# Performance work log

Measured on AMD Instinct MI355X. Metric: run time of the kernel, lower is better.

## Reference

```python
import jax, jax.numpy as jnp
import numpy as np

SIG = [1, 1, 1, 1, -1]  # Cl(4,1)
NVEC = 5
GA = 1 << NVEC  # 32


def _build_gp_table():
    # Cayley table for the geometric product on blades indexed by bitmask.
    G = np.zeros((GA, GA, GA), np.float32)
    for a in range(GA):
        for b in range(GA):
            s = 0
            t = a >> 1
            while t:
                s += bin(t & b).count('1')
                t >>= 1
            sign = -1.0 if (s & 1) else 1.0
            common = a & b
            for i in range(NVEC):
                if (common >> i) & 1:
                    sign *= SIG[i]
            G[a, b, a ^ b] = sign
    return G

GP_TABLE = jnp.asarray(_build_gp_table())


def geometric_product(x, y):
    return jnp.einsum('...i,...j,ijk->...k', x, y, GP_TABLE)


def manifold_norm(x):
    # normalize each multivector onto the unit sphere in R^32
    return x / (jnp.linalg.norm(x, axis=-1, keepdims=True) + 1e-6)


def versor_linear(x, W, b):
    # channel mixing shared across multivector components: x [..., in, ga]
    return jnp.einsum('...ig,oi->...og', x, W) + b


def layer_norm2d(x, w, b):
    # LayerNorm over last two dims [D, ga] jointly
    mu = jnp.mean(x, axis=(-2, -1), keepdims=True)
    var = jnp.var(x, axis=(-2, -1), keepdims=True)
    return (x - mu) / jnp.sqrt(var + 1e-5) * w + b


def attention(x, Wq, bq, Wk, bk, Wv, bv, Wo, bo, n_heads):
    B, S, D, G = x.shape
    dh = D // n_heads
    q = versor_linear(x, Wq, bq).reshape(B, S, n_heads, dh, G)
    k = versor_linear(x, Wk, bk).reshape(B, S, n_heads, dh, G)
    v = versor_linear(x, Wv, bv).reshape(B, S, n_heads, dh, G)
    scale = 1.0 / np.sqrt(dh * G).astype(np.float32)
    scores = jnp.einsum('bshdg,bthdg->bhst', q, k) * scale
    probs = jax.nn.softmax(scores, axis=-1)
    o = jnp.einsum('bhst,bthdg->bshdg', probs, v).reshape(B, S, D, G)
    return versor_linear(o, Wo, bo)


N_HEADS = 8


def forward(x, Wq, bq, Wk, bk, Wv, bv, Wo, bo, ln1_w, ln1_b, ln2_w, ln2_b,
            gamma1, gamma2, W1, b1, W2, b2, Wr, br, Wc, bc):
    L = Wq.shape[0]
    for l in range(L):
        h = attention(layer_norm2d(x, ln1_w[l], ln1_b[l]),
                      Wq[l], bq[l], Wk[l], bk[l], Wv[l], bv[l], Wo[l], bo[l], N_HEADS)
        x = manifold_norm(x + gamma1[l] * h)
        m = versor_linear(layer_norm2d(x, ln2_w[l], ln2_b[l]), W1[l], b1[l])
        m = versor_linear(jnp.tanh(m), W2[l], b2[l])
        x = manifold_norm(x + gamma2[l] * m)
    # RecursiveRotorAccumulator: log(S)-step inclusive scan of rotors
    delta = versor_linear(x, Wr, br)
    rot = 0.5 * delta
    rot = rot.at[..., 0].add(1.0)
    rot = manifold_norm(rot)
    S = x.shape[1]
    step = 1
    while step < S:
        left = rot[:, :-step]
        right = rot[:, step:]
        comb = manifold_norm(geometric_product(right, left))
        rot = jnp.concatenate([rot[:, :step], comb], axis=1)
        step *= 2
    pooled = rot[:, -1]  # [B, D, ga]
    logits = pooled.reshape(pooled.shape[0], -1) @ Wc.T + bc
    return logits


def setup_inputs() -> dict:
    key = jax.random.key(0)
    B, S, D, G, L, NC = 8, 256, 64, GA, 4, 1000
    E = 4 * D  # expansion hidden
    ks = jax.random.split(key, 16)
    sd = 0.02
    inp = {
        'x': jax.random.normal(ks[0], (B, S, D, G), jnp.float32),
        'Wq': jax.random.normal(ks[1], (L, D, D), jnp.float32) * sd,
        'bq': jnp.zeros((L, D, G), jnp.float32),
        'Wk': jax.random.normal(ks[2], (L, D, D), jnp.float32) * sd,
        'bk': jnp.zeros((L, D, G), jnp.float32),
        'Wv': jax.random.normal(ks[3], (L, D, D), jnp.float32) * sd,
        'bv': jnp.zeros((L, D, G), jnp.float32),
        'Wo': jax.random.normal(ks[4], (L, D, D), jnp.float32) * sd,
        'bo': jnp.zeros((L, D, G), jnp.float32),
        'ln1_w': jnp.ones((L, D, G), jnp.float32),
        'ln1_b': jnp.zeros((L, D, G), jnp.float32),
        'ln2_w': jnp.ones((L, D, G), jnp.float32),
        'ln2_b': jnp.zeros((L, D, G), jnp.float32),
        'gamma1': 1e-5 * jnp.ones((L, D, G), jnp.float32),
        'gamma2': 1e-5 * jnp.ones((L, D, G), jnp.float32),
        'W1': jax.random.normal(ks[5], (L, E, D), jnp.float32) * sd,
        'b1': jnp.zeros((L, E, G), jnp.float32),
        'W2': jax.random.normal(ks[6], (L, D, E), jnp.float32) * sd,
        'b2': jnp.zeros((L, D, G), jnp.float32),
        'Wr': jax.random.normal(ks[7], (D, D), jnp.float32) * sd,
        'br': jnp.zeros((D, G), jnp.float32),
        'Wc': jax.random.normal(ks[8], (NC, D * G), jnp.float32) * sd,
        'bc': jnp.zeros((NC,), jnp.float32),
    }
    return inp


def reference(x, Wq, bq, Wk, bk, Wv, bv, Wo, bo, ln1_w, ln1_b, ln2_w, ln2_b,
              gamma1, gamma2, W1, b1, W2, b2, Wr, br, Wc, bc):
    return forward(x, Wq, bq, Wk, bk, Wv, bv, Wo, bo, ln1_w, ln1_b, ln2_w, ln2_b,
                   gamma1, gamma2, W1, b1, W2, b2, Wr, br, Wc, bc)
```

## Files before the change

kernel.cpp:

```cpp
#include <hip/hip_runtime.h>
#include <hip/hip_bf16.h>

constexpr int kB  = 8;
constexpr int kS  = 256;
constexpr int kD  = 64;
constexpr int kG  = 32;
constexpr int kE  = 256;
constexpr int kNH = 8;
constexpr int kHD = 256;
constexpr int kDG = kD * kG;
constexpr int kT  = kB * kS;
constexpr int kNC = 1000;

using bf16x8 = __attribute__((ext_vector_type(8))) short;
using f32x4  = __attribute__((ext_vector_type(4))) float;

__device__ __forceinline__ short f2bf(float f) {
    unsigned u = __float_as_uint(f);
    unsigned r = (u + 0x7FFFu + ((u >> 16) & 1u)) >> 16;
    return (short)r;
}

__device__ __forceinline__ float tanh_fast(float x) {
    float a = fabsf(x);
    float e = __expf(-2.f * a);
    float d = 1.f + e;
    float r = __builtin_amdgcn_rcpf(d);
    r = r * (2.f - d * r);
    float t = (1.f - e) * r;
    return copysignf(t, x);
}

__global__ __launch_bounds__(256) void cvtw_kernel(
    const float* __restrict__ Wq, const float* __restrict__ Wk,
    const float* __restrict__ Wv, const float* __restrict__ Wo,
    const float* __restrict__ W1, const float* __restrict__ W2,
    unsigned short* __restrict__ dst) {
    int idx = (blockIdx.x * 256 + threadIdx.x) * 4;
    const float* src; int off;
    if      (idx <  16384) { src = Wq; off = 0; }
    else if (idx <  32768) { src = Wk; off = 16384; }
    else if (idx <  49152) { src = Wv; off = 32768; }
    else if (idx <  65536) { src = Wo; off = 49152; }
    else if (idx < 131072) { src = W1; off = 65536; }
    else                   { src = W2; off = 131072; }
    const float4 v = *(const float4*)(src + (idx - off));
    *(short4*)&dst[idx] = make_short4(f2bf(v.x), f2bf(v.y), f2bf(v.z), f2bf(v.w));
}

__global__ __launch_bounds__(256) void prep_tr_kernel(
    const float* __restrict__ bq, const float* __restrict__ bk,
    const float* __restrict__ bv, const float* __restrict__ bo,
    const float* __restrict__ b2, const float* __restrict__ gm1,
    const float* __restrict__ gm2, const float* __restrict__ ln2w,
    const float* __restrict__ ln2b, const float* __restrict__ ln1w,
    const float* __restrict__ ln1b, const float* __restrict__ b1,
    float* __restrict__ dst) {
    __shared__ float lt[32 * 257];
    const int a = blockIdx.x >> 2, l = blockIdx.x & 3;
    const float* srcs[12] = {bq, bk, bv, bo, b2, gm1, gm2, ln2w, ln2b, ln1w, ln1b, b1};
    const int R  = (a == 11) ? 256 : 64;
    const int sh = (a == 11) ? 8 : 6;
    const float* src = srcs[a] + (size_t)l * R * 32;
    float* out = dst + a * 8192 + l * R * 32;
    const int tid = threadIdx.x;
    for (int j = tid; j < R * 32; j += 256) lt[(j & 31) * (R + 1) + (j >> 5)] = src[j];
    __syncthreads();
    for (int k = tid; k < R * 32; k += 256) {
        int g = k >> sh, r = k & (R - 1);
        out[k] = lt[g * (R + 1) + r];
    }
}

__global__ __launch_bounds__(256) void ln_kernel(const float* __restrict__ Xin,
                                                 const float* __restrict__ w,
                                                 const float* __restrict__ b,
                                                 unsigned short* __restrict__ A,
                                                 float* __restrict__ XT) {
    int t = blockIdx.x, tid = threadIdx.x;
    const float* xp = Xin + (size_t)t * kDG;
    __shared__ float r1[256], r2[256];
    __shared__ short st[32 * 72];
    __shared__ float xf[32 * 68];
    float v[8], s = 0.f, ss = 0.f;
#pragma unroll
    for (int j = 0; j < 8; j++) {
        float x = xp[tid + j * 256];
        v[j] = x; s += x; ss += x * x;
        int jj = tid + j * 256;
        xf[(jj & 31) * 68 + (jj >> 5)] = x;
    }
    r1[tid] = s; r2[tid] = ss; __syncthreads();
    for (int o = 128; o > 0; o >>= 1) {
        if (tid < o) { r1[tid] += r1[tid + o]; r2[tid] += r2[tid + o]; }
        __syncthreads();
    }
    float mean = r1[0] * (1.f / kDG);
    float var  = r2[0] * (1.f / kDG) - mean * mean;
    float rstd = rsqrtf(var + 1e-5f);
#pragma unroll
    for (int j = 0; j < 8; j++) {
        int jj = tid + j * 256;
        float val = (v[j] - mean) * rstd * w[jj] + b[jj];
        st[(jj & 31) * 72 + (jj >> 5)] = f2bf(val);
    }
    __syncthreads();
    bf16x8 ov = *(const bf16x8*)&st[(tid >> 3) * 72 + (tid & 7) * 8];
    *(bf16x8*)&A[(size_t)t * kDG + tid * 8] = ov;
    const int row = tid >> 3, col = (tid & 7) * 8;
    float* xo = XT + (size_t)t * kDG + tid * 8;
    *(float4*)(xo + 0) = *(const float4*)&xf[row * 68 + col + 0];
    *(float4*)(xo + 4) = *(const float4*)&xf[row * 68 + col + 4];
}

__global__ __launch_bounds__(256) void vlinT_kernel(const float* __restrict__ XT,
                                                    const float* __restrict__ W,
                                                    const float* __restrict__ bias,
                                                    float* __restrict__ OutT) {
    __shared__ float sx[32 * 65];
    __shared__ float sw[kD * kD];
    int t = blockIdx.x, tid = threadIdx.x;
    const float* xp = XT + (size_t)t * kDG;
    for (int j = tid; j < kDG; j += 256) sx[(j >> 6) * 65 + (j & 63)] = xp[j];
    for (int j = tid; j < kD * kD; j += 256) sw[j] = W[j];
    __syncthreads();
    int g = tid & 31, ob = tid >> 5;
    int b = t >> 8, s = t & 255;
    float* op = OutT + ((size_t)b * kD * kS + s) * kG;
    for (int o = ob; o < kD; o += 8) {
        float acc = bias[o * kG + g];
        const float* wr = sw + o * kD;
#pragma unroll
        for (int i = 0; i < kD; i++) acc += wr[i] * sx[g * 65 + i];
        op[(size_t)o * kS * kG + g] = acc;
    }
}

template<bool LAST>
__global__ __launch_bounds__(256, 2) void mega_kernel(
    const unsigned short* __restrict__ O,
    const unsigned short* __restrict__ Woh, const float* __restrict__ boT,
    const float* __restrict__ gm1T,
    const float* __restrict__ ln2wT, const float* __restrict__ ln2bT,
    const unsigned short* __restrict__ W1h, const float* __restrict__ b1T,
    const unsigned short* __restrict__ W2h, const float* __restrict__ b2T,
    const float* __restrict__ gm2T,
    const float* __restrict__ ln1wT, const float* __restrict__ ln1bT,
    float* __restrict__ XT,
    const unsigned short* __restrict__ Wqh, const unsigned short* __restrict__ Wkh,
    const unsigned short* __restrict__ Wvh,
    const float* __restrict__ bqT, const float* __restrict__ bkT,
    const float* __restrict__ bvT,
    unsigned short* __restrict__ Q, unsigned short* __restrict__ K,
    unsigned short* __restrict__ V) {
    constexpr int AS = 72;
    constexpr int MS = 264;
    __shared__ short sA[32 * AS];
    __shared__ short sM[32 * MS];
    __shared__ float sred[8];

    const int tid = threadIdx.x;
    const int w = tid >> 6, lane = tid & 63;
    const int l16 = lane & 15, quad = lane >> 4;
    const int tok = blockIdx.x;
    const size_t tb = (size_t)tok * kDG;
    const int o0 = w * 16 + quad * 4;

    float xv[2][4];
    bf16x8 w1f[8];
    {
        const unsigned short* xp = O + tb;
        bf16x8 bfr[2][2];
#pragma unroll
        for (int c = 0; c < 2; ++c)
#pragma unroll
            for (int nt = 0; nt < 2; ++nt)
                bfr[c][nt] = *(const bf16x8*)&xp[(nt * 16 + l16) * kD + c * 32 + quad * 8];

        f32x4 accW[2];
#pragma unroll
        for (int nt = 0; nt < 2; ++nt) accW[nt] = (f32x4){0.f, 0.f, 0.f, 0.f};
#pragma unroll
        for (int c = 0; c < 2; ++c) {
            bf16x8 afr = *(const bf16x8*)&Woh[(w * 16 + l16) * kD + c * 32 + quad * 8];
#pragma unroll
            for (int nt = 0; nt < 2; ++nt)
                accW[nt] = __builtin_amdgcn_mfma_f32_16x16x32_bf16(afr, bfr[c][nt], accW[nt], 0, 0, 0);
        }

#pragma unroll
        for (int mt = 0; mt < 4; ++mt)
#pragma unroll
            for (int c = 0; c < 2; ++c)
                w1f[mt * 2 + c] = *(const bf16x8*)&W1h[((w * 4 + mt) * 16 + l16) * kD + c * 32 + quad * 8];

        float4 lw2[2], lb2[2];
#pragma unroll
        for (int nt = 0; nt < 2; ++nt) {
            int g = nt * 16 + l16;
            lw2[nt] = *(const float4*)&ln2wT[g * kD + o0];
            lb2[nt] = *(const float4*)&ln2bT[g * kD + o0];
        }

        float s = 0.f, ss = 0.f;
        float vv[2][4];
#pragma unroll
        for (int nt = 0; nt < 2; ++nt) {
            int g = nt * 16 + l16;
            const float4 b4 = *(const float4*)&boT[g * kD + o0];
            const float4 g4 = *(const float4*)&gm1T[g * kD + o0];
            const float4 xi = *(const float4*)&XT[tb + g * kD + o0];
#pragma unroll
            for (int r = 0; r < 4; ++r)
                vv[nt][r] = (&xi.x)[r] + (&g4.x)[r] * (accW[nt][r] + (&b4.x)[r]);
        }
#pragma unroll
        for (int r = 0; r < 4; ++r) {
            float sq = vv[0][r] * vv[0][r] + vv[1][r] * vv[1][r];
#pragma unroll
            for (int off = 1; off < 16; off <<= 1) sq += __shfl_xor(sq, off, 64);
            float rn = 1.f / (sqrtf(sq) + 1e-6f);
#pragma unroll
            for (int nt = 0; nt < 2; ++nt) {
                float x = vv[nt][r] * rn;
                xv[nt][r] = x;
                s += x; ss = fmaf(x, x, ss);
            }
        }
#pragma unroll
        for (int off = 1; off < 64; off <<= 1) {
            s += __shfl_xor(s, off, 64); ss += __shfl_xor(ss, off, 64);
        }
        if (lane == 0) { sred[w] = s; sred[4 + w] = ss; }
        __syncthreads();
        float st = sred[0] + sred[1] + sred[2] + sred[3];
        float sst = sred[4] + sred[5] + sred[6] + sred[7];
        float mean = st * (1.f / kDG);
        float var  = sst * (1.f / kDG) - mean * mean;
        float rstd = rsqrtf(var + 1e-5f);
#pragma unroll
        for (int nt = 0; nt < 2; ++nt) {
            int g = nt * 16 + l16;
            short4 s4;
#pragma unroll
            for (int r = 0; r < 4; ++r)
                (&s4.x)[r] = f2bf((xv[nt][r] - mean) * rstd * (&lw2[nt].x)[r] + (&lb2[nt].x)[r]);
            *(short4*)&sA[g * AS + o0] = s4;
        }
    }
    __syncthreads();

    bf16x8 w2f[8];
    {
        bf16x8 afrA[2][2];
#pragma unroll
        for (int c = 0; c < 2; ++c)
#pragma unroll
            for (int nt = 0; nt < 2; ++nt)
                afrA[c][nt] = *(const bf16x8*)&sA[(nt * 16 + l16) * AS + c * 32 + quad * 8];

        f32x4 acc1[4][2];
#pragma unroll
        for (int mt = 0; mt < 4; ++mt)
#pragma unroll
            for (int nt = 0; nt < 2; ++nt) acc1[mt][nt] = (f32x4){0.f, 0.f, 0.f, 0.f};
#pragma unroll
        for (int mt = 0; mt < 4; ++mt)
#pragma unroll
            for (int c = 0; c < 2; ++c)
#pragma unroll
                for (int nt = 0; nt < 2; ++nt)
                    acc1[mt][nt] = __builtin_amdgcn_mfma_f32_16x16x32_bf16(w1f[mt * 2 + c], afrA[c][nt], acc1[mt][nt], 0, 0, 0);

#pragma unroll
        for (int c = 0; c < 8; ++c)
            w2f[c] = *(const bf16x8*)&W2h[(w * 16 + l16) * kE + c * 32 + quad * 8];

#pragma unroll
        for (int mt = 0; mt < 4; ++mt)
#pragma unroll
            for (int nt = 0; nt < 2; ++nt) {
                int g = nt * 16 + l16;
                int e0 = (w * 4 + mt) * 16 + quad * 4;
                const float4 b4 = *(const float4*)&b1T[g * kE + e0];
                short4 s4;
#pragma unroll
                for (int r = 0; r < 4; ++r)
                    (&s4.x)[r] = f2bf(tanh_fast(acc1[mt][nt][r] + (&b4.x)[r]));
                *(short4*)&sM[g * MS + e0] = s4;
            }
    }
    __syncthreads();

    f32x4 acc2[2];
#pragma unroll
    for (int nt = 0; nt < 2; ++nt) acc2[nt] = (f32x4){0.f, 0.f, 0.f, 0.f};
#pragma unroll
    for (int c = 0; c < 8; ++c) {
        bf16x8 bq[2];
#pragma unroll
        for (int nt = 0; nt < 2; ++nt)
            bq[nt] = *(const bf16x8*)&sM[(nt * 16 + l16) * MS + c * 32 + quad * 8];
#pragma unroll
        for (int nt = 0; nt < 2; ++nt)
            acc2[nt] = __builtin_amdgcn_mfma_f32_16x16x32_bf16(w2f[c], bq[nt], acc2[nt], 0, 0, 0);
    }

    bf16x8 wqf[6];
    float4 lw1[2], lb1[2], pbq[2], pbk[2], pbv[2];
    if constexpr (!LAST) {
        const unsigned short* Wp[3] = {Wqh, Wkh, Wvh};
#pragma unroll
        for (int m = 0; m < 3; ++m)
#pragma unroll
            for (int c = 0; c < 2; ++c)
                wqf[m * 2 + c] = *(const bf16x8*)&Wp[m][(w * 16 + l16) * kD + c * 32 + quad * 8];
#pragma unroll
        for (int nt = 0; nt < 2; ++nt) {
            int g = nt * 16 + l16;
            lw1[nt] = *(const float4*)&ln1wT[g * kD + o0];
            lb1[nt] = *(const float4*)&ln1bT[g * kD + o0];
            pbq[nt] = *(const float4*)&bqT[g * kD + o0];
            pbk[nt] = *(const float4*)&bkT[g * kD + o0];
            pbv[nt] = *(const float4*)&bvT[g * kD + o0];
        }
    }

    float yv[2][4];
    float s2 = 0.f, ss2 = 0.f;
    {
        float vv[2][4];
#pragma unroll
        for (int nt = 0; nt < 2; ++nt) {
            int g = nt * 16 + l16;
            const float4 b4 = *(const float4*)&b2T[g * kD + o0];
            const float4 g4 = *(const float4*)&gm2T[g * kD + o0];
#pragma unroll
            for (int r = 0; r < 4; ++r)
                vv[nt][r] = xv[nt][r] + (&g4.x)[r] * (acc2[nt][r] + (&b4.x)[r]);
        }
#pragma unroll
        for (int r = 0; r < 4; ++r) {
            float sq = vv[0][r] * vv[0][r] + vv[1][r] * vv[1][r];
#pragma unroll
            for (int off = 1; off < 16; off <<= 1) sq += __shfl_xor(sq, off, 64);
            float rn = 1.f / (sqrtf(sq) + 1e-6f);
#pragma unroll
            for (int nt = 0; nt < 2; ++nt) {
                float x = vv[nt][r] * rn;
                yv[nt][r] = x;
                s2 += x; ss2 = fmaf(x, x, ss2);
            }
        }
#pragma unroll
        for (int nt = 0; nt < 2; ++nt) {
            int g = nt * 16 + l16;
            float4 xo;
#pragma unroll
            for (int r = 0; r < 4; ++r) (&xo.x)[r] = yv[nt][r];
            *(float4*)&XT[tb + g * kD + o0] = xo;
        }
    }
    if constexpr (LAST) return;

#pragma unroll
    for (int off = 1; off < 64; off <<= 1) {
        s2 += __shfl_xor(s2, off, 64); ss2 += __shfl_xor(ss2, off, 64);
    }
    if (lane == 0) { sred[w] = s2; sred[4 + w] = ss2; }
    __syncthreads();
    {
        float st = sred[0] + sred[1] + sred[2] + sred[3];
        float sst = sred[4] + sred[5] + sred[6] + sred[7];
        float mean = st * (1.f / kDG);
        float var  = sst * (1.f / kDG) - mean * mean;
        float rstd = rsqrtf(var + 1e-5f);
#pragma unroll
        for (int nt = 0; nt < 2; ++nt) {
            int g = nt * 16 + l16;
            short4 s4;
#pragma unroll
            for (int r = 0; r < 4; ++r)
                (&s4.x)[r] = f2bf((yv[nt][r] - mean) * rstd * (&lw1[nt].x)[r] + (&lb1[nt].x)[r]);
            *(short4*)&sA[g * AS + o0] = s4;
        }
    }
    __syncthreads();

    {
        bf16x8 afrA[2][2];
#pragma unroll
        for (int c = 0; c < 2; ++c)
#pragma unroll
            for (int nt = 0; nt < 2; ++nt)
                afrA[c][nt] = *(const bf16x8*)&sA[(nt * 16 + l16) * AS + c * 32 + quad * 8];

        const float4* Bp[3][2] = {{&pbq[0], &pbq[1]}, {&pbk[0], &pbk[1]}, {&pbv[0], &pbv[1]}};
        unsigned short* Op[3] = {Q, K, V};
#pragma unroll
        for (int m = 0; m < 3; ++m) {
            f32x4 acc3[2];
#pragma unroll
            for (int nt = 0; nt < 2; ++nt) acc3[nt] = (f32x4){0.f, 0.f, 0.f, 0.f};
#pragma unroll
            for (int c = 0; c < 2; ++c)
#pragma unroll
                for (int nt = 0; nt < 2; ++nt)
                    acc3[nt] = __builtin_amdgcn_mfma_f32_16x16x32_bf16(wqf[m * 2 + c], afrA[c][nt], acc3[nt], 0, 0, 0);
            unsigned short* op = Op[m] + tb;
#pragma unroll
            for (int nt = 0; nt < 2; ++nt) {
                int g = nt * 16 + l16;
                const float4 b4 = *Bp[m][nt];
#pragma unroll
                for (int r = 0; r < 4; ++r)
                    op[(o0 + r) * kG + g] = (unsigned short)f2bf(acc3[nt][r] + (&b4.x)[r]);
            }
        }
    }
}

__global__ __launch_bounds__(256, 3) void gemm_qkv_kernel(
    const unsigned short* __restrict__ X,
    const unsigned short* __restrict__ Wqh, const unsigned short* __restrict__ Wkh,
    const unsigned short* __restrict__ Wvh,
    const float* __restrict__ bqT, const float* __restrict__ bkT, const float* __restrict__ bvT,
    unsigned short* __restrict__ Q, unsigned short* __restrict__ K, unsigned short* __restrict__ V) {
    constexpr int WS = 64 + 8;
    __shared__ short sW[3 * 64 * WS];

    const int tid = threadIdx.x, wave = tid >> 6, lane = tid & 63;
    const int l16 = lane & 15, quad = lane >> 4;
    const int tok = blockIdx.x * 4 + wave;

    const unsigned short* Wp[3] = {Wqh, Wkh, Wvh};
#pragma unroll
    for (int w = 0; w < 3; ++w)
        for (int j = tid * 8; j < 64 * 64; j += 2048) {
            int o = j >> 6, i = j & 63;
            *(bf16x8*)&sW[w * 64 * WS + o * WS + i] = *(const bf16x8*)(Wp[w] + j);
        }

    const unsigned short* xp = X + (size_t)tok * kDG;
    bf16x8 bfr[2][2];
#pragma unroll
    for (int c = 0; c < 2; ++c)
#pragma unroll
        for (int nt = 0; nt < 2; ++nt)
            bfr[c][nt] = *(const bf16x8*)&xp[(nt * 16 + l16) * kD + c * 32 + quad * 8];
    __syncthreads();

    f32x4 acc[3][4][2];
#pragma unroll
    for (int w = 0; w < 3; ++w)
#pragma unroll
        for (int mt = 0; mt < 4; ++mt)
#pragma unroll
            for (int nt = 0; nt < 2; ++nt) acc[w][mt][nt] = (f32x4){0.f, 0.f, 0.f, 0.f};

#pragma unroll
    for (int w = 0; w < 3; ++w)
#pragma unroll
        for (int mt = 0; mt < 4; ++mt)
#pragma unroll
            for (int c = 0; c < 2; ++c) {
                bf16x8 afr = *(const bf16x8*)&sW[w * 64 * WS + (mt * 16 + l16) * WS + c * 32 + quad * 8];
#pragma unroll
                for (int nt = 0; nt < 2; ++nt)
                    acc[w][mt][nt] = __builtin_amdgcn_mfma_f32_16x16x32_bf16(afr, bfr[c][nt], acc[w][mt][nt], 0, 0, 0);
            }

    unsigned short* Op[3] = {Q, K, V};
    const float* Bp[3] = {bqT, bkT, bvT};
#pragma unroll
    for (int w = 0; w < 3; ++w) {
        unsigned short* op = Op[w] + (size_t)tok * kDG;
#pragma unroll
        for (int mt = 0; mt < 4; ++mt)
#pragma unroll
            for (int nt = 0; nt < 2; ++nt) {
                int g = nt * 16 + l16;
                int o0 = mt * 16 + quad * 4;
                const float4 b4 = *(const float4*)&Bp[w][g * kD + o0];
#pragma unroll
                for (int r = 0; r < 4; ++r)
                    op[(o0 + r) * kG + g] = (unsigned short)f2bf(acc[w][mt][nt][r] + (&b4.x)[r]);
            }
    }
}

constexpr int QSTR = 264;
constexpr int VSTR = 40;

__global__ __launch_bounds__(128) void attn_mfma_kernel(const unsigned short* __restrict__ Q,
                                                        const unsigned short* __restrict__ K,
                                                        const unsigned short* __restrict__ V,
                                                        unsigned short* __restrict__ O) {
    __shared__ short sP[32 * QSTR];
    __shared__ short sKV[2][256 * VSTR];

    const int qt = blockIdx.x, h = blockIdx.y, b = blockIdx.z;
    const int tid = threadIdx.x;
    const int wave = tid >> 6, lane = tid & 63;
    const int l16 = lane & 15, quad = lane >> 4;

    const size_t bh = (size_t)b * kS * kDG + (size_t)h * kHD;

    bf16x8 afrag[8];
    {
        const unsigned short* qp = Q + bh + (size_t)(qt * 32 + wave * 16 + l16) * kDG;
#pragma unroll
        for (int c = 0; c < 8; ++c)
            afrag[c] = *(const bf16x8*)(qp + c * 32 + quad * 8);
    }

#pragma unroll
    for (int it = 0; it < 8; ++it) {
        int j = it * 1024 + tid * 8;
        int row = j >> 8, col = j & 255;
        *(bf16x8*)&sKV[0][row * QSTR + col] =
            *(const bf16x8*)(K + bh + (size_t)row * kDG + col);
    }
    __syncthreads();

    f32x4 acc[16];
#pragma unroll
    for (int i = 0; i < 16; ++i) acc[i] = (f32x4){0.f, 0.f, 0.f, 0.f};

    for (int kt = 0; kt < 8; ++kt) {
        bf16x8 kpre[8];
        if (kt < 7) {
#pragma unroll
            for (int it = 0; it < 8; ++it) {
                int j = it * 1024 + tid * 8;
                int row = j >> 8, col = j & 255;
                kpre[it] = *(const bf16x8*)(K + bh + (size_t)((kt + 1) * 32 + row) * kDG + col);
            }
        }
        const short* kb = sKV[kt & 1];
#pragma unroll
        for (int nt = 0; nt < 2; ++nt) {
            int key = nt * 16 + l16;
            f32x4 a = acc[kt * 2 + nt];
#pragma unroll
            for (int c = 0; c < 8; ++c) {
                bf16x8 bfrag = *(const bf16x8*)&kb[key * QSTR + c * 32 + quad * 8];
                a = __builtin_amdgcn_mfma_f32_16x16x32_bf16(afrag[c], bfrag, a, 0, 0, 0);
            }
            acc[kt * 2 + nt] = a;
        }
        if (kt < 7) {
            short* nb = sKV[(kt + 1) & 1];
#pragma unroll
            for (int it = 0; it < 8; ++it) {
                int j = it * 1024 + tid * 8;
                int row = j >> 8, col = j & 255;
                *(bf16x8*)&nb[row * QSTR + col] = kpre[it];
            }
            __syncthreads();
        }
    }

    float inv[4];
#pragma unroll
    for (int r = 0; r < 4; ++r) {
        float m = -1e30f;
#pragma unroll
        for (int t = 0; t < 16; ++t) m = fmaxf(m, acc[t][r]);
#pragma unroll
        for (int off = 1; off < 16; off <<= 1) m = fmaxf(m, __shfl_xor(m, off, 16));
        float s = 0.f;
#pragma unroll
        for (int t = 0; t < 16; ++t) {
            float p = __expf((acc[t][r] - m) * 0.0625f);
            acc[t][r] = p; s += p;
        }
#pragma unroll
        for (int off = 1; off < 16; off <<= 1) s += __shfl_xor(s, off, 16);
        inv[r] = 1.f / s;
    }

#pragma unroll
    for (int t = 0; t < 16; ++t)
#pragma unroll
        for (int r = 0; r < 4; ++r)
            sP[(wave * 16 + quad * 4 + r) * QSTR + t * 16 + l16] = f2bf(acc[t][r]);

    {
        const int db = tid & 63, kh = tid >> 6;
        short4 vr[16];
#pragma unroll
        for (int r = 0; r < 16; ++r)
            vr[r] = *(const short4*)(V + bh + (size_t)(kh * 16 + r) * kDG + db * 4);
#pragma unroll
        for (int i = 0; i < 4; ++i)
#pragma unroll
            for (int gq = 0; gq < 4; ++gq) {
                short4 p = make_short4((&vr[gq * 4 + 0].x)[i], (&vr[gq * 4 + 1].x)[i],
                                       (&vr[gq * 4 + 2].x)[i], (&vr[gq * 4 + 3].x)[i]);
                *(short4*)&sKV[0][(db * 4 + i) * VSTR + kh * 16 + gq * 4] = p;
            }
    }
    __syncthreads();

    f32x4 oacc[16];
#pragma unroll
    for (int i = 0; i < 16; ++i) oacc[i] = (f32x4){0.f, 0.f, 0.f, 0.f};

    for (int vt = 0; vt < 8; ++vt) {
        short4 vpre[16];
        if (vt < 7) {
            const int db = tid & 63, kh = tid >> 6;
#pragma unroll
            for (int r = 0; r < 16; ++r)
                vpre[r] = *(const short4*)(V + bh + (size_t)((vt + 1) * 32 + kh * 16 + r) * kDG + db * 4);
        }
        const short* vb = sKV[vt & 1];
        bf16x8 pfrag = *(const bf16x8*)&sP[(wave * 16 + l16) * QSTR + vt * 32 + quad * 8];
#pragma unroll
        for (int dt = 0; dt < 16; ++dt) {
            bf16x8 vfrag = *(const bf16x8*)&vb[(dt * 16 + l16) * VSTR + quad * 8];
            oacc[dt] = __builtin_amdgcn_mfma_f32_16x16x32_bf16(pfrag, vfrag, oacc[dt], 0, 0, 0);
        }
        if (vt < 7) {
            const int db = tid & 63, kh = tid >> 6;
            short* nb = sKV[(vt + 1) & 1];
#pragma unroll
            for (int i = 0; i < 4; ++i)
#pragma unroll
                for (int gq = 0; gq < 4; ++gq) {
                    short4 p = make_short4((&vpre[gq * 4 + 0].x)[i], (&vpre[gq * 4 + 1].x)[i],
                                           (&vpre[gq * 4 + 2].x)[i], (&vpre[gq * 4 + 3].x)[i]);
                    *(short4*)&nb[(db * 4 + i) * VSTR + kh * 16 + gq * 4] = p;
                }
            __syncthreads();
        }
    }

    {
        const size_t ob = (size_t)(b * kS + qt * 32 + wave * 16 + quad * 4) * kDG + h * 8;
#pragma unroll
        for (int gg = 0; gg < 2; ++gg) {
            int g = gg * 16 + l16;
#pragma unroll
            for (int r = 0; r < 4; ++r) {
                bf16x8 pk;
#pragma unroll
                for (int k = 0; k < 8; ++k)
                    pk[k] = f2bf(oacc[k * 2 + gg][r] * inv[r]);
                *(bf16x8*)&O[ob + (size_t)r * kDG + g * kD] = pk;
            }
        }
    }
}

constexpr int pc_ce(unsigned v) { int c = 0; while (v) { c += v & 1; v >>= 1; } return c; }
constexpr unsigned gp_mask_ce(int a) {
    unsigned m = 0;
    for (int c = 0; c < 32; ++c) {
        int b = a ^ c;
        int s = (a & b) >> 4;
        for (int t = a >> 1; t; t >>= 1) s += pc_ce(t & b);
        if (s & 1) m |= (1u << c);
    }
    return m;
}

template<int A>
__device__ __forceinline__ void gp_term(const float* x, const float* y, float* acc) {
    constexpr unsigned m = gp_mask_ce(A);
    const float xa = x[A], nxa = -xa;
#pragma unroll
    for (int c = 0; c < 32; ++c)
        acc[c] = fmaf(((m >> c) & 1u) ? nxa : xa, y[A ^ c], acc[c]);
}

__device__ __forceinline__ void gp_mn_t(const float* x, const float* y, float* out) {
    float acc[32];
#pragma unroll
    for (int c = 0; c < 32; ++c) acc[c] = 0.f;
    gp_term<0>(x, y, acc);  gp_term<1>(x, y, acc);  gp_term<2>(x, y, acc);  gp_term<3>(x, y, acc);
    gp_term<4>(x, y, acc);  gp_term<5>(x, y, acc);  gp_term<6>(x, y, acc);  gp_term<7>(x, y, acc);
    gp_term<8>(x, y, acc);  gp_term<9>(x, y, acc);  gp_term<10>(x, y, acc); gp_term<11>(x, y, acc);
    gp_term<12>(x, y, acc); gp_term<13>(x, y, acc); gp_term<14>(x, y, acc); gp_term<15>(x, y, acc);
    gp_term<16>(x, y, acc); gp_term<17>(x, y, acc); gp_term<18>(x, y, acc); gp_term<19>(x, y, acc);
    gp_term<20>(x, y, acc); gp_term<21>(x, y, acc); gp_term<22>(x, y, acc); gp_term<23>(x, y, acc);
    gp_term<24>(x, y, acc); gp_term<25>(x, y, acc); gp_term<26>(x, y, acc); gp_term<27>(x, y, acc);
    gp_term<28>(x, y, acc); gp_term<29>(x, y, acc); gp_term<30>(x, y, acc); gp_term<31>(x, y, acc);
    float ss = 0.f;
#pragma unroll
    for (int c = 0; c < 32; ++c) ss = fmaf(acc[c], acc[c], ss);
    float r = 1.f / (sqrtf(ss) + 1e-6f);
#pragma unroll
    for (int c = 0; c < 32; ++c) out[c] = acc[c] * r;
}

__device__ __forceinline__ void leaf_load(const float* base, float* v) {
#pragma unroll
    for (int i = 0; i < 8; ++i) {
        const float4 f = *(const float4*)(base + i * 4);
        v[i * 4 + 0] = 0.5f * f.x; v[i * 4 + 1] = 0.5f * f.y;
        v[i * 4 + 2] = 0.5f * f.z; v[i * 4 + 3] = 0.5f * f.w;
    }
    v[0] += 1.f;
    float ss = 0.f;
#pragma unroll
    for (int c = 0; c < 32; ++c) ss = fmaf(v[c], v[c], ss);
    float r = 1.f / (sqrtf(ss) + 1e-6f);
#pragma unroll
    for (int c = 0; c < 32; ++c) v[c] *= r;
}

__global__ __launch_bounds__(64) void scanreg_kernel(const float* __restrict__ DT,
                                                     float* __restrict__ pooled) {
    const int lane = threadIdx.x & 63;
    const int seq = blockIdx.x;
    const float* base = DT + ((size_t)seq * kS + lane * 4) * kG;

    float R[32], Y[32], P[32], Xa[32], Yb[32];

    leaf_load(base, R);
    for (int j = 1; j < 4; ++j) {
        leaf_load(base + j * kG, Y);
        gp_mn_t(Y, R, R);
    }

    for (int step = 1; step < 64; step <<= 1) {
        const bool up = lane & step;
#pragma unroll
        for (int c = 0; c < 32; ++c) P[c] = __shfl_xor(R[c], step, 64);
#pragma unroll
        for (int c = 0; c < 32; ++c) {
            Xa[c] = up ? R[c] : P[c];
            Yb[c] = up ? P[c] : R[c];
        }
        gp_mn_t(Xa, Yb, R);
    }

    if (lane == 0) {
        float* op = pooled + (size_t)seq * kG;
#pragma unroll
        for (int i = 0; i < 8; ++i)
            *(float4*)(op + i * 4) = make_float4(R[i * 4], R[i * 4 + 1], R[i * 4 + 2], R[i * 4 + 3]);
    }
}

__global__ __launch_bounds__(256) void cls2_kernel(const float* __restrict__ P,
                                                   const float* __restrict__ Wc,
                                                   const float* __restrict__ bc,
                                                   float* __restrict__ out) {
    __shared__ float sp[kB * kDG];
    const int tid = threadIdx.x, wave = tid >> 6, lane = tid & 63;
    for (int j = tid * 4; j < kB * kDG; j += 1024)
        *(float4*)&sp[j] = *(const float4*)(P + j);
    __syncthreads();

    const int c = blockIdx.x * 4 + wave;
    const float* w = Wc + (size_t)c * kDG;
    float acc[kB];
#pragma unroll
    for (int b = 0; b < kB; ++b) acc[b] = 0.f;
#pragma unroll
    for (int cc = 0; cc < 8; ++cc) {
        const float4 w4 = *(const float4*)(w + cc * 256 + lane * 4);
#pragma unroll
        for (int b = 0; b < kB; ++b) {
            const float4 p4 = *(const float4*)&sp[b * kDG + cc * 256 + lane * 4];
            acc[b] += w4.x * p4.x + w4.y * p4.y + w4.z * p4.z + w4.w * p4.w;
        }
    }
#pragma unroll
    for (int b = 0; b < kB; ++b)
#pragma unroll
        for (int off = 32; off > 0; off >>= 1) acc[b] += __shfl_xor(acc[b], off, 64);
    if (lane == 0) {
        float bias = bc[c];
#pragma unroll
        for (int b = 0; b < kB; ++b) out[b * kNC + c] = acc[b] + bias;
    }
}

extern "C" void kernel_launch(void* const* d_in, const int* in_sizes, int n_in,
                              void* d_out, int out_size, void* d_ws, size_t ws_size,
                              hipStream_t stream) {
    const float* x_in = (const float*)d_in[0];
    const float* Wq   = (const float*)d_in[1];
    const float* bq   = (const float*)d_in[2];
    const float* Wk   = (const float*)d_in[3];
    const float* bk   = (const float*)d_in[4];
    const float* Wv   = (const float*)d_in[5];
    const float* bv   = (const float*)d_in[6];
    const float* Wo   = (const float*)d_in[7];
    const float* bo   = (const float*)d_in[8];
    const float* ln1w = (const float*)d_in[9];
    const float* ln1b = (const float*)d_in[10];
    const float* ln2w = (const float*)d_in[11];
    const float* ln2b = (const float*)d_in[12];
    const float* gm1  = (const float*)d_in[13];
    const float* gm2  = (const float*)d_in[14];
    const float* W1   = (const float*)d_in[15];
    const float* b1   = (const float*)d_in[16];
    const float* W2   = (const float*)d_in[17];
    const float* b2   = (const float*)d_in[18];
    const float* Wr   = (const float*)d_in[19];
    const float* br   = (const float*)d_in[20];
    const float* Wc   = (const float*)d_in[21];
    const float* bc   = (const float*)d_in[22];

    const size_t NEL = (size_t)kT * kDG;
    float* F  = (float*)d_ws;
    float* XT = F;
    unsigned short* Abf = (unsigned short*)(F + NEL);
    unsigned short* Qh = (unsigned short*)(F + 2 * NEL);
    unsigned short* Kh = (unsigned short*)(F + 3 * NEL);
    unsigned short* Vh = (unsigned short*)(F + 4 * NEL);
    unsigned short* Wb = (unsigned short*)(F + 5 * NEL);
    float* PT = F + 3 * NEL + NEL / 2;
    float* pooled = F + 2 * NEL;
    float* DT = F + NEL;

    cvtw_kernel<<<192, 256, 0, stream>>>(Wq, Wk, Wv, Wo, W1, W2, Wb);
    prep_tr_kernel<<<48, 256, 0, stream>>>(bq, bk, bv, bo, b2, gm1, gm2,
                                           ln2w, ln2b, ln1w, ln1b, b1, PT);
    unsigned short* Wqh = Wb;
    unsigned short* Wkh = Wb + 16384;
    unsigned short* Wvh = Wb + 32768;
    unsigned short* Woh = Wb + 49152;
    unsigned short* W1h = Wb + 65536;
    unsigned short* W2h = Wb + 131072;

    auto bqT   = [&](int l) { return PT + 0     + l * 2048; };
    auto bkT   = [&](int l) { return PT + 8192  + l * 2048; };
    auto bvT   = [&](int l) { return PT + 16384 + l * 2048; };
    auto boT   = [&](int l) { return PT + 24576 + l * 2048; };
    auto b2T   = [&](int l) { return PT + 32768 + l * 2048; };
    auto gm1T  = [&](int l) { return PT + 40960 + l * 2048; };
    auto gm2T  = [&](int l) { return PT + 49152 + l * 2048; };
    auto ln2wT = [&](int l) { return PT + 57344 + l * 2048; };
    auto ln2bT = [&](int l) { return PT + 65536 + l * 2048; };
    auto ln1wT = [&](int l) { return PT + 73728 + l * 2048; };
    auto ln1bT = [&](int l) { return PT + 81920 + l * 2048; };
    auto b1T   = [&](int l) { return PT + 90112 + l * 8192; };

    ln_kernel<<<kT, 256, 0, stream>>>(x_in, ln1w, ln1b, Abf, XT);
    gemm_qkv_kernel<<<kT / 4, 256, 0, stream>>>(Abf,
        Wqh, Wkh, Wvh, bqT(0), bkT(0), bvT(0), Qh, Kh, Vh);

    for (int l = 0; l < 4; l++) {
        attn_mfma_kernel<<<dim3(8, kNH, kB), 128, 0, stream>>>(Qh, Kh, Vh, Abf);
        if (l < 3)
            mega_kernel<false><<<kT, 256, 0, stream>>>(Abf,
                Woh + l * 4096, boT(l), gm1T(l), ln2wT(l), ln2bT(l),
                W1h + l * 16384, b1T(l), W2h + l * 16384, b2T(l), gm2T(l),
                ln1wT(l + 1), ln1bT(l + 1), XT,
                Wqh + (l + 1) * 4096, Wkh + (l + 1) * 4096, Wvh + (l + 1) * 4096,
                bqT(l + 1), bkT(l + 1), bvT(l + 1), Qh, Kh, Vh);
        else
            mega_kernel<true><<<kT, 256, 0, stream>>>(Abf,
                Woh + l * 4096, boT(l), gm1T(l), ln2wT(l), ln2bT(l),
                W1h + l * 16384, b1T(l), W2h + l * 16384, b2T(l), gm2T(l),
                nullptr, nullptr, XT,
                nullptr, nullptr, nullptr, nullptr, nullptr, nullptr,
                nullptr, nullptr, nullptr);
    }

    vlinT_kernel<<<kT, 256, 0, stream>>>(XT, Wr, br, DT);
    scanreg_kernel<<<kB * kD, 64, 0, stream>>>(DT, pooled);
    cls2_kernel<<<kNC / 4, 256, 0, stream>>>(pooled, Wc, bc, (float*)d_out);
}
```

Before: 510.2 us.

## Process two tokens per block in mega_kernel to reuse weight fragments

Each mega_kernel block now handles two tokens instead of one. The Wo, W1, W2 and QKV weight fragments, plus the per-position bias, gamma and layernorm vectors, are loaded into registers once and applied to both tokens, halving weight traffic per token. Shared buffers are doubled and the grid is halved. Launch bounds are raised from 2 to 4 blocks per CU, which tightens the register budget for a kernel that now keeps more live state and may cause spills.

```diff
diff --git a/kernel.cpp b/kernel.cpp
--- a/kernel.cpp
+++ b/kernel.cpp
@@ -137,7 +137,7 @@
 }
 
 template<bool LAST>
-__global__ __launch_bounds__(256, 2) void mega_kernel(
+__global__ __launch_bounds__(256, 4) void mega_kernel(
     const unsigned short* __restrict__ O,
     const unsigned short* __restrict__ Woh, const float* __restrict__ boT,
     const float* __restrict__ gm1T,
@@ -155,37 +155,42 @@
     unsigned short* __restrict__ V) {
     constexpr int AS = 72;
     constexpr int MS = 264;
-    __shared__ short sA[32 * AS];
-    __shared__ short sM[32 * MS];
-    __shared__ float sred[8];
+    __shared__ short sA[2][32 * AS];
+    __shared__ short sM[2][32 * MS];
+    __shared__ float sred[2][8];
 
     const int tid = threadIdx.x;
     const int w = tid >> 6, lane = tid & 63;
     const int l16 = lane & 15, quad = lane >> 4;
-    const int tok = blockIdx.x;
-    const size_t tb = (size_t)tok * kDG;
+    const size_t tb0 = (size_t)(blockIdx.x * 2) * kDG;
+    const size_t tbs[2] = {tb0, tb0 + kDG};
     const int o0 = w * 16 + quad * 4;
 
-    float xv[2][4];
+    float xv[2][2][4];
     bf16x8 w1f[8];
+
     {
-        const unsigned short* xp = O + tb;
-        bf16x8 bfr[2][2];
+        bf16x8 wof[2];
 #pragma unroll
         for (int c = 0; c < 2; ++c)
-#pragma unroll
-            for (int nt = 0; nt < 2; ++nt)
-                bfr[c][nt] = *(const bf16x8*)&xp[(nt * 16 + l16) * kD + c * 32 + quad * 8];
-
-        f32x4 accW[2];
-#pragma unroll
-        for (int nt = 0; nt < 2; ++nt) accW[nt] = (f32x4){0.f, 0.f, 0.f, 0.f};
-#pragma unroll
-        for (int c = 0; c < 2; ++c) {
-            bf16x8 afr = *(const bf16x8*)&Woh[(w * 16 + l16) * kD + c * 32 + quad * 8];
-#pragma unroll
-            for (int nt = 0; nt < 2; ++nt)
-                accW[nt] = __builtin_amdgcn_mfma_f32_16x16x32_bf16(afr, bfr[c][nt], accW[nt], 0, 0, 0);
+            wof[c] = *(const bf16x8*)&Woh[(w * 16 + l16) * kD + c * 32 + quad * 8];
+
+        f32x4 accW[2][2];
+#pragma unroll
+        for (int t = 0; t < 2; ++t) {
+            bf16x8 bfr[2][2];
+#pragma unroll
+            for (int c = 0; c < 2; ++c)
+#pragma unroll
+                for (int nt = 0; nt < 2; ++nt)
+                    bfr[c][nt] = *(const bf16x8*)&O[tbs[t] + (nt * 16 + l16) * kD + c * 32 + quad * 8];
+#pragma unroll
+            for (int nt = 0; nt < 2; ++nt) accW[t][nt] = (f32x4){0.f, 0.f, 0.f, 0.f};
+#pragma unroll
+            for (int c = 0; c < 2; ++c)
+#pragma unroll
+                for (int nt = 0; nt < 2; ++nt)
+                    accW[t][nt] = __builtin_amdgcn_mfma_f32_16x16x32_bf16(wof[c], bfr[c][nt], accW[t][nt], 0, 0, 0);
         }
 
 #pragma unroll
@@ -194,70 +199,83 @@
             for (int c = 0; c < 2; ++c)
                 w1f[mt * 2 + c] = *(const bf16x8*)&W1h[((w * 4 + mt) * 16 + l16) * kD + c * 32 + quad * 8];
 
-        float4 lw2[2], lb2[2];
+        float s[2] = {0.f, 0.f}, ssq[2] = {0.f, 0.f};
+        float4 b4[2], g4[2], lw2[2], lb2[2];
 #pragma unroll
         for (int nt = 0; nt < 2; ++nt) {
             int g = nt * 16 + l16;
+            b4[nt]  = *(const float4*)&boT[g * kD + o0];
+            g4[nt]  = *(const float4*)&gm1T[g * kD + o0];
             lw2[nt] = *(const float4*)&ln2wT[g * kD + o0];
             lb2[nt] = *(const float4*)&ln2bT[g * kD + o0];
         }
-
-        float s = 0.f, ss = 0.f;
-        float vv[2][4];
-#pragma unroll
-        for (int nt = 0; nt < 2; ++nt) {
-            int g = nt * 16 + l16;
-            const float4 b4 = *(const float4*)&boT[g * kD + o0];
-            const float4 g4 = *(const float4*)&gm1T[g * kD + o0];
-            const float4 xi = *(const float4*)&XT[tb + g * kD + o0];
-#pragma unroll
-            for (int r = 0; r < 4; ++r)
-                vv[nt][r] = (&xi.x)[r] + (&g4.x)[r] * (accW[nt][r] + (&b4.x)[r]);
-        }
-#pragma unroll
-        for (int r = 0; r < 4; ++r) {
-            float sq = vv[0][r] * vv[0][r] + vv[1][r] * vv[1][r];
-#pragma unroll
-            for (int off = 1; off < 16; off <<= 1) sq += __shfl_xor(sq, off, 64);
-            float rn = 1.f / (sqrtf(sq) + 1e-6f);
+#pragma unroll
+        for (int t = 0; t < 2; ++t) {
+            float vv[2][4];
 #pragma unroll
             for (int nt = 0; nt < 2; ++nt) {
-                float x = vv[nt][r] * rn;
-                xv[nt][r] = x;
-                s += x; ss = fmaf(x, x, ss);
+                int g = nt * 16 + l16;
+                const float4 xi = *(const float4*)&XT[tbs[t] + g * kD + o0];
+#pragma unroll
+                for (int r = 0; r < 4; ++r)
+                    vv[nt][r] = (&xi.x)[r] + (&g4[nt].x)[r] * (accW[t][nt][r] + (&b4[nt].x)[r]);
+            }
+#pragma unroll
+            for (int r = 0; r < 4; ++r) {
+                float sq = vv[0][r] * vv[0][r] + vv[1][r] * vv[1][r];
+#pragma unroll
+                for (int off = 1; off < 16; off <<= 1) sq += __shfl_xor(sq, off, 64);
+                float rn = 1.f / (sqrtf(sq) + 1e-6f);
+#pragma unroll
+                for (int nt = 0; nt < 2; ++nt) {
+                    float x = vv[nt][r] * rn;
+                    xv[t][nt][r] = x;
+                    s[t] += x; ssq[t] = fmaf(x, x, ssq[t]);
+                }
             }
         }
 #pragma unroll
         for (int off = 1; off < 64; off <<= 1) {
-            s += __shfl_xor(s, off, 64); ss += __shfl_xor(ss, off, 64);
-        }
-        if (lane == 0) { sred[w] = s; sred[4 + w] = ss; }
+#pragma unroll
+            for (int t = 0; t < 2; ++t) {
+                s[t] += __shfl_xor(s[t], off, 64);
+                ssq[t] += __shfl_xor(ssq[t], off, 64);
+            }
+        }
+        if (lane == 0) {
+#pragma unroll
+            for (int t = 0; t < 2; ++t) { sred[t][w] = s[t]; sred[t][4 + w] = ssq[t]; }
+        }
         __syncthreads();
-        float st = sred[0] + sred[1] + sred[2] + sred[3];
-        float sst = sred[4] + sred[5] + sred[6] + sred[7];
-        float mean = st * (1.f / kDG);
-        float var  = sst * (1.f / kDG) - mean * mean;
-        float rstd = rsqrtf(var + 1e-5f);
-#pragma unroll
-        for (int nt = 0; nt < 2; ++nt) {
-            int g = nt * 16 + l16;
-            short4 s4;
-#pragma unroll
-            for (int r = 0; r < 4; ++r)
-                (&s4.x)[r] = f2bf((xv[nt][r] - mean) * rstd * (&lw2[nt].x)[r] + (&lb2[nt].x)[r]);
-            *(short4*)&sA[g * AS + o0] = s4;
+#pragma unroll
+        for (int t = 0; t < 2; ++t) {
+            float st = sred[t][0] + sred[t][1] + sred[t][2] + sred[t][3];
+            float sst = sred[t][4] + sred[t][5] + sred[t][6] + sred[t][7];
+            float mean = st * (1.f / kDG);
+            float var  = sst * (1.f / kDG) - mean * mean;
+            float rstd = rsqrtf(var + 1e-5f);
+#pragma unroll
+            for (int nt = 0; nt < 2; ++nt) {
+                int g = nt * 16 + l16;
+                short4 s4;
+#pragma unroll
+                for (int r = 0; r < 4; ++r)
+                    (&s4.x)[r] = f2bf((xv[t][nt][r] - mean) * rstd * (&lw2[nt].x)[r] + (&lb2[nt].x)[r]);
+                *(short4*)&sA[t][g * AS + o0] = s4;
+            }
         }
     }
     __syncthreads();
 
     bf16x8 w2f[8];
-    {
+#pragma unroll
+    for (int t = 0; t < 2; ++t) {
         bf16x8 afrA[2][2];
 #pragma unroll
         for (int c = 0; c < 2; ++c)
 #pragma unroll
             for (int nt = 0; nt < 2; ++nt)
-                afrA[c][nt] = *(const bf16x8*)&sA[(nt * 16 + l16) * AS + c * 32 + quad * 8];
+                afrA[c][nt] = *(const bf16x8*)&sA[t][(nt * 16 + l16) * AS + c * 32 + quad * 8];
 
         f32x4 acc1[4][2];
 #pragma unroll
@@ -272,9 +290,11 @@
                 for (int nt = 0; nt < 2; ++nt)
                     acc1[mt][nt] = __builtin_amdgcn_mfma_f32_16x16x32_bf16(w1f[mt * 2 + c], afrA[c][nt], acc1[mt][nt], 0, 0, 0);
 
-#pragma unroll
-        for (int c = 0; c < 8; ++c)
-            w2f[c] = *(const bf16x8*)&W2h[(w * 16 + l16) * kE + c * 32 + quad * 8];
+        if (t == 0) {
+#pragma unroll
+            for (int c = 0; c < 8; ++c)
+                w2f[c] = *(const bf16x8*)&W2h[(w * 16 + l16) * kE + c * 32 + quad * 8];
+        }
 
 #pragma unroll
         for (int mt = 0; mt < 4; ++mt)
@@ -287,27 +307,31 @@
 #pragma unroll
                 for (int r = 0; r < 4; ++r)
                     (&s4.x)[r] = f2bf(tanh_fast(acc1[mt][nt][r] + (&b4.x)[r]));
-                *(short4*)&sM[g * MS + e0] = s4;
+                *(short4*)&sM[t][g * MS + e0] = s4;
             }
     }
     __syncthreads();
 
-    f32x4 acc2[2];
-#pragma unroll
-    for (int nt = 0; nt < 2; ++nt) acc2[nt] = (f32x4){0.f, 0.f, 0.f, 0.f};
+    f32x4 acc2[2][2];
+#pragma unroll
+    for (int t = 0; t < 2; ++t)
+#pragma unroll
+        for (int nt = 0; nt < 2; ++nt) acc2[t][nt] = (f32x4){0.f, 0.f, 0.f, 0.f};
 #pragma unroll
     for (int c = 0; c < 8; ++c) {
-        bf16x8 bq[2];
-#pragma unroll
-        for (int nt = 0; nt < 2; ++nt)
-            bq[nt] = *(const bf16x8*)&sM[(nt * 16 + l16) * MS + c * 32 + quad * 8];
-#pragma unroll
-        for (int nt = 0; nt < 2; ++nt)
-            acc2[nt] = __builtin_amdgcn_mfma_f32_16x16x32_bf16(w2f[c], bq[nt], acc2[nt], 0, 0, 0);
+#pragma unroll
+        for (int t = 0; t < 2; ++t) {
+            bf16x8 bq[2];
+#pragma unroll
+            for (int nt = 0; nt < 2; ++nt)
+                bq[nt] = *(const bf16x8*)&sM[t][(nt * 16 + l16) * MS + c * 32 + quad * 8];
+#pragma unroll
+            for (int nt = 0; nt < 2; ++nt)
+                acc2[t][nt] = __builtin_amdgcn_mfma_f32_16x16x32_bf16(w2f[c], bq[nt], acc2[t][nt], 0, 0, 0);
+        }
     }
 
     bf16x8 wqf[6];
-    float4 lw1[2], lb1[2], pbq[2], pbk[2], pbv[2];
     if constexpr (!LAST) {
         const unsigned short* Wp[3] = {Wqh, Wkh, Wvh};
 #pragma unroll
@@ -315,106 +339,120 @@
 #pragma unroll
             for (int c = 0; c < 2; ++c)
                 wqf[m * 2 + c] = *(const bf16x8*)&Wp[m][(w * 16 + l16) * kD + c * 32 + quad * 8];
+    }
+
+    {
+        float s2[2] = {0.f, 0.f}, ssq2[2] = {0.f, 0.f};
+        float yv[2][2][4];
+        float4 b4[2], g4[2];
+#pragma unroll
+        for (int nt = 0; nt < 2; ++nt) {
+            int g = nt * 16 + l16;
+            b4[nt] = *(const float4*)&b2T[g * kD + o0];
+            g4[nt] = *(const float4*)&gm2T[g * kD + o0];
+        }
+#pragma unroll
+        for (int t = 0; t < 2; ++t) {
+            float vv[2][4];
+#pragma unroll
+            for (int nt = 0; nt < 2; ++nt)
+#pragma unroll
+                for (int r = 0; r < 4; ++r)
+                    vv[nt][r] = xv[t][nt][r] + (&g4[nt].x)[r] * (acc2[t][nt][r] + (&b4[nt].x)[r]);
+#pragma unroll
+            for (int r = 0; r < 4; ++r) {
+                float sq = vv[0][r] * vv[0][r] + vv[1][r] * vv[1][r];
+#pragma unroll
+                for (int off = 1; off < 16; off <<= 1) sq += __shfl_xor(sq, off, 64);
+                float rn = 1.f / (sqrtf(sq) + 1e-6f);
+#pragma unroll
+                for (int nt = 0; nt < 2; ++nt) {
+                    float x = vv[nt][r] * rn;
+                    yv[t][nt][r] = x;
+                    s2[t] += x; ssq2[t] = fmaf(x, x, ssq2[t]);
+                }
+            }
+#pragma unroll
+            for (int nt = 0; nt < 2; ++nt) {
+                int g = nt * 16 + l16;
+                float4 xo;
+#pragma unroll
+                for (int r = 0; r < 4; ++r) (&xo.x)[r] = yv[t][nt][r];
+                *(float4*)&XT[tbs[t] + g * kD + o0] = xo;
+            }
+        }
+        if constexpr (LAST) return;
+
+#pragma unroll
+        for (int off = 1; off < 64; off <<= 1) {
+#pragma unroll
+            for (int t = 0; t < 2; ++t) {
+                s2[t] += __shfl_xor(s2[t], off, 64);
+                ssq2[t] += __shfl_xor(ssq2[t], off, 64);
+            }
+        }
+        if (lane == 0) {
+#pragma unroll
+            for (int t = 0; t < 2; ++t) { sred[t][w] = s2[t]; sred[t][4 + w] = ssq2[t]; }
+        }
+        __syncthreads();
+        float4 lw1[2], lb1[2];
 #pragma unroll
         for (int nt = 0; nt < 2; ++nt) {
             int g = nt * 16 + l16;
             lw1[nt] = *(const float4*)&ln1wT[g * kD + o0];
             lb1[nt] = *(const float4*)&ln1bT[g * kD + o0];
-            pbq[nt] = *(const float4*)&bqT[g * kD + o0];
-            pbk[nt] = *(const float4*)&bkT[g * kD + o0];
-            pbv[nt] = *(const float4*)&bvT[g * kD + o0];
-        }
-    }
-
-    float yv[2][4];
-    float s2 = 0.f, ss2 = 0.f;
-    {
-        float vv[2][4];
-#pragma unroll
-        for (int nt = 0; nt < 2; ++nt) {
-            int g = nt * 16 + l16;
-            const float4 b4 = *(const float4*)&b2T[g * kD + o0];
-            const float4 g4 = *(const float4*)&gm2T[g * kD + o0];
-#pragma unroll
-            for (int r = 0; r < 4; ++r)
-                vv[nt][r] = xv[nt][r] + (&g4.x)[r] * (acc2[nt][r] + (&b4.x)[r]);
-        }
-#pragma unroll
-        for (int r = 0; r < 4; ++r) {
-            float sq = vv[0][r] * vv[0][r] + vv[1][r] * vv[1][r];
-#pragma unroll
-            for (int off = 1; off < 16; off <<= 1) sq += __shfl_xor(sq, off, 64);
-            float rn = 1.f / (sqrtf(sq) + 1e-6f);
-#pragma unroll
-            for (int nt = 0; nt < 2; ++nt) {
-                float x = vv[nt][r] * rn;
-                yv[nt][r] = x;
-                s2 += x; ss2 = fmaf(x, x, ss2);
-            }
-        }
-#pragma unroll
-        for (int nt = 0; nt < 2; ++nt) {
-            int g = nt * 16 + l16;
-            float4 xo;
-#pragma unroll
-            for (int r = 0; r < 4; ++r) (&xo.x)[r] = yv[nt][r];
-            *(float4*)&XT[tb + g * kD + o0] = xo;
-        }
-    }
-    if constexpr (LAST) return;
-
-#pragma unroll
-    for (int off = 1; off < 64; off <<= 1) {
-        s2 += __shfl_xor(s2, off, 64); ss2 += __shfl_xor(ss2, off, 64);
-    }
-    if (lane == 0) { sred[w] = s2; sred[4 + w] = ss2; }
-    __syncthreads();
-    {
-        float st = sred[0] + sred[1] + sred[2] + sred[3];
-        float sst = sred[4] + sred[5] + sred[6] + sred[7];
-        float mean = st * (1.f / kDG);
-        float var  = sst * (1.f / kDG) - mean * mean;
-        float rstd = rsqrtf(var + 1e-5f);
-#pragma unroll
-        for (int nt = 0; nt < 2; ++nt) {
-            int g = nt * 16 + l16;
-            short4 s4;
-#pragma unroll
-            for (int r = 0; r < 4; ++r)
-                (&s4.x)[r] = f2bf((yv[nt][r] - mean) * rstd * (&lw1[nt].x)[r] + (&lb1[nt].x)[r]);
-            *(short4*)&sA[g * AS + o0] = s4;
-        }
-    }
-    __syncthreads();
-
-    {
-        bf16x8 afrA[2][2];
-#pragma unroll
-        for (int c = 0; c < 2; ++c)
-#pragma unroll
-            for (int nt = 0; nt < 2; ++nt)
-                afrA[c][nt] = *(const bf16x8*)&sA[(nt * 16 + l16) * AS + c * 32 + quad * 8];
-
-        const float4* Bp[3][2] = {{&pbq[0], &pbq[1]}, {&pbk[0], &pbk[1]}, {&pbv[0], &pbv[1]}};
-        unsigned short* Op[3] = {Q, K, V};
-#pragma unroll
-        for (int m = 0; m < 3; ++m) {
-            f32x4 acc3[2];
-#pragma unroll
-            for (int nt = 0; nt < 2; ++nt) acc3[nt] = (f32x4){0.f, 0.f, 0.f, 0.f};
-#pragma unroll
-            for (int c = 0; c < 2; ++c)
-#pragma unroll
-                for (int nt = 0; nt < 2; ++nt)
-                    acc3[nt] = __builtin_amdgcn_mfma_f32_16x16x32_bf16(wqf[m * 2 + c], afrA[c][nt], acc3[nt], 0, 0, 0);
-            unsigned short* op = Op[m] + tb;
+        }
+#pragma unroll
+        for (int t = 0; t < 2; ++t) {
+            float st = sred[t][0] + sred[t][1] + sred[t][2] + sred[t][3];
+            float sst = sred[t][4] + sred[t][5] + sred[t][6] + sred[t][7];
+            float mean = st * (1.f / kDG);
+            float var  = sst * (1.f / kDG) - mean * mean;
+            float rstd = rsqrtf(var + 1e-5f);
 #pragma unroll
             for (int nt = 0; nt < 2; ++nt) {
                 int g = nt * 16 + l16;
-                const float4 b4 = *Bp[m][nt];
+                short4 s4;
 #pragma unroll
                 for (int r = 0; r < 4; ++r)
-                    op[(o0 + r) * kG + g] = (unsigned short)f2bf(acc3[nt][r] + (&b4.x)[r]);
+                    (&s4.x)[r] = f2bf((yv[t][nt][r] - mean) * rstd * (&lw1[nt].x)[r] + (&lb1[nt].x)[r]);
+                *(short4*)&sA[t][g * AS + o0] = s4;
+            }
+        }
+    }
+    __syncthreads();
+
+    if constexpr (!LAST) {
+        const float* Bp[3] = {bqT, bkT, bvT};
+        unsigned short* Op[3] = {Q, K, V};
+#pragma unroll
+        for (int t = 0; t < 2; ++t) {
+            bf16x8 afrA[2][2];
+#pragma unroll
+            for (int c = 0; c < 2; ++c)
+#pragma unroll
+                for (int nt = 0; nt < 2; ++nt)
+                    afrA[c][nt] = *(const bf16x8*)&sA[t][(nt * 16 + l16) * AS + c * 32 + quad * 8];
+#pragma unroll
+            for (int m = 0; m < 3; ++m) {
+                f32x4 acc3[2];
+#pragma unroll
+                for (int nt = 0; nt < 2; ++nt) acc3[nt] = (f32x4){0.f, 0.f, 0.f, 0.f};
+#pragma unroll
+                for (int c = 0; c < 2; ++c)
+#pragma unroll
+                    for (int nt = 0; nt < 2; ++nt)
+                        acc3[nt] = __builtin_amdgcn_mfma_f32_16x16x32_bf16(wqf[m * 2 + c], afrA[c][nt], acc3[nt], 0, 0, 0);
+                unsigned short* op = Op[m] + tbs[t];
+#pragma unroll
+                for (int nt = 0; nt < 2; ++nt) {
+                    int g = nt * 16 + l16;
+                    const float4 b4 = *(const float4*)&Bp[m][g * kD + o0];
+#pragma unroll
+                    for (int r = 0; r < 4; ++r)
+                        op[(o0 + r) * kG + g] = (unsigned short)f2bf(acc3[nt][r] + (&b4.x)[r]);
+                }
             }
         }
     }
@@ -849,14 +887,14 @@
     for (int l = 0; l < 4; l++) {
         attn_mfma_kernel<<<dim3(8, kNH, kB), 128, 0, stream>>>(Qh, Kh, Vh, Abf);
         if (l < 3)
-            mega_kernel<false><<<kT, 256, 0, stream>>>(Abf,
+            mega_kernel<false><<<kT / 2, 256, 0, stream>>>(Abf,
                 Woh + l * 4096, boT(l), gm1T(l), ln2wT(l), ln2bT(l),
                 W1h + l * 16384, b1T(l), W2h + l * 16384, b2T(l), gm2T(l),
                 ln1wT(l + 1), ln1bT(l + 1), XT,
                 Wqh + (l + 1) * 4096, Wkh + (l + 1) * 4096, Wvh + (l + 1) * 4096,
                 bqT(l + 1), bkT(l + 1), bvT(l + 1), Qh, Kh, Vh);
         else
-            mega_kernel<true><<<kT, 256, 0, stream>>>(Abf,
+            mega_kernel<true><<<kT / 2, 256, 0, stream>>>(Abf,
                 Woh + l * 4096, boT(l), gm1T(l), ln2wT(l), ln2bT(l),
                 W1h + l * 16384, b1T(l), W2h + l * 16384, b2T(l), gm2T(l),
                 nullptr, nullptr, XT,
```

New measurement: 527.1 us. +3.3%, slower.
